# Performance work log

Hardware: AMD Instinct MI355X
Metric: run time of the kernel (lower is better)

The kernel has to match this reference:

```python
import jax, jax.numpy as jnp
import numpy as np

T, H, I, E, K = 4096, 1024, 768, 8, 2

def setup_inputs() -> dict:
    key = jax.random.key(0)
    k1, k2, k3, k4 = jax.random.split(key, 4)
    s_h = 1.0 / np.sqrt(H)
    s_i = 1.0 / np.sqrt(I)
    return {
        "hidden_states": jax.random.normal(k1, (T, H), dtype=jnp.float32),
        "gate_w": jax.random.normal(k2, (E, H), dtype=jnp.float32) * s_h,   # router, fp32
        "w13": jax.random.normal(k3, (E, 2 * I, H), dtype=jnp.float32) * s_h,  # fused gate+up
        "w2": jax.random.normal(k4, (E, H, I), dtype=jnp.float32) * s_i,
        "num_global_tokens": T,
        "max_num_tokens_per_gpu": T,
    }

def reference(hidden_states, gate_w, w13, w2, num_global_tokens, max_num_tokens_per_gpu):
    x = hidden_states  # [T, H]
    orig_dtype = x.dtype
    # router runs in fp32 (router_dtype == 'float32')
    router_logits = jnp.einsum('th,eh->te', x.astype(jnp.float32), gate_w)
    router_logits = router_logits.astype(orig_dtype)
    # FusedMoE top-k: softmax in fp32 over all experts, then top-k; renormalize=False
    probs = jax.nn.softmax(router_logits.astype(jnp.float32), axis=-1)  # [T, E]
    topk_w, topk_ids = jax.lax.top_k(probs, K)  # [T, K]
    # dense combine weights [T, E] (scatter of top-k weights)
    combine = jnp.sum(jax.nn.one_hot(topk_ids, E, dtype=topk_w.dtype) * topk_w[..., None], axis=1)
    combine = combine.astype(orig_dtype)
    # dense per-expert SwiGLU MLP, masked-combined (grouped GEMM reference)
    h = jnp.einsum('th,ejh->tej', x, w13)  # [T, E, 2I]
    g, u = h[..., :I], h[..., I:]
    a = jax.nn.silu(g) * u                 # [T, E, I]
    o = jnp.einsum('tei,ehi->teh', a, w2)  # [T, E, H]
    out = jnp.einsum('teh,te->th', o, combine)  # routed_scaling_factor = 1.0
    return out.reshape(x.shape)
```

## Files before the change

### kernel.cpp

```cpp
#include <hip/hip_runtime.h>
#include <hip/hip_bf16.h>

#define TT 4096
#define HH 1024
#define II 768
#define EE 8
#define TWOI 1536

typedef __attribute__((ext_vector_type(8))) short bf16x8;
typedef __attribute__((ext_vector_type(4))) float f32x4;

__device__ unsigned short g_x_bf[TT * HH];
__device__ unsigned short g_w13_bf[EE * TWOI * HH];
__device__ unsigned short g_w2_bf[EE * HH * II];
__device__ unsigned short g_a[EE * TT * II];
__device__ float g_opart[2 * TT * HH];
__device__ int g_perm_tok[EE * TT];
__device__ float g_perm_w[EE * TT];
__device__ int g_perm_slot[EE * TT];
__device__ int g_cnt[EE];
__device__ int g_e1[TT];
__device__ int g_e2[TT];
__device__ float g_w1f[TT];
__device__ float g_w2f[TT];

__device__ __forceinline__ unsigned short f2bf(float f) {
  union { float f; unsigned u; } v; v.f = f;
  unsigned r = v.u + 0x7fff + ((v.u >> 16) & 1);
  return (unsigned short)(r >> 16);
}

__device__ __forceinline__ void gload16(const void* g, void* l) {
  __builtin_amdgcn_global_load_lds(
      (const __attribute__((address_space(1))) void*)g,
      (__attribute__((address_space(3))) void*)l, 16, 0, 0);
}

__device__ __forceinline__ void cvt_chunks(const float* __restrict__ in,
                                           unsigned short* __restrict__ dst,
                                           int nKB, int chunk) {
  const int lane = threadIdx.x & 63;
  const int r16 = lane & 15, c8 = lane >> 4;
  const int jbg = chunk / nKB, kb = chunk - jbg * nKB;
  const float* src = in + ((size_t)jbg * 16 + r16) * ((size_t)nKB * 32) + kb * 32 + c8 * 8;
  float4 v0 = *(const float4*)(src);
  float4 v1 = *(const float4*)(src + 4);
  ushort4 o0, o1;
  o0.x = f2bf(v0.x); o0.y = f2bf(v0.y); o0.z = f2bf(v0.z); o0.w = f2bf(v0.w);
  o1.x = f2bf(v1.x); o1.y = f2bf(v1.y); o1.z = f2bf(v1.z); o1.w = f2bf(v1.w);
  unsigned short* d = dst + (size_t)chunk * 512 + lane * 8;
  *(ushort4*)(d) = o0;
  *(ushort4*)(d + 4) = o1;
}

__global__ __launch_bounds__(256) void k_prep(const float* __restrict__ x,
                                              const float* __restrict__ gw,
                                              const float* __restrict__ w13) {
  const int b = blockIdx.x;
  const int wv = threadIdx.x >> 6;
  if (b >= 1024) {
    cvt_chunks(w13, g_w13_bf, 32, (b - 1024) * 4 + wv);
    return;
  }
  const int lane = threadIdx.x & 63;
  const int t = b * 4 + wv;

  const float* xr = x + (size_t)t * HH + lane * 16;
  float4 xv0 = *(const float4*)(xr + 0);
  float4 xv1 = *(const float4*)(xr + 4);
  float4 xv2 = *(const float4*)(xr + 8);
  float4 xv3 = *(const float4*)(xr + 12);

  unsigned short* xd = g_x_bf + (size_t)t * HH + lane * 16;
  ushort4 o0, o1, o2, o3;
  o0.x = f2bf(xv0.x); o0.y = f2bf(xv0.y); o0.z = f2bf(xv0.z); o0.w = f2bf(xv0.w);
  o1.x = f2bf(xv1.x); o1.y = f2bf(xv1.y); o1.z = f2bf(xv1.z); o1.w = f2bf(xv1.w);
  o2.x = f2bf(xv2.x); o2.y = f2bf(xv2.y); o2.z = f2bf(xv2.z); o2.w = f2bf(xv2.w);
  o3.x = f2bf(xv3.x); o3.y = f2bf(xv3.y); o3.z = f2bf(xv3.z); o3.w = f2bf(xv3.w);
  *(ushort4*)(xd + 0) = o0;
  *(ushort4*)(xd + 4) = o1;
  *(ushort4*)(xd + 8) = o2;
  *(ushort4*)(xd + 12) = o3;

  float lg[EE];
#pragma unroll
  for (int ei = 0; ei < EE; ++ei) {
    const float* gr = gw + ei * HH + lane * 16;
    float4 g0 = *(const float4*)(gr + 0);
    float4 g1 = *(const float4*)(gr + 4);
    float4 g2 = *(const float4*)(gr + 8);
    float4 g3 = *(const float4*)(gr + 12);
    float a = xv0.x * g0.x + xv0.y * g0.y + xv0.z * g0.z + xv0.w * g0.w
            + xv1.x * g1.x + xv1.y * g1.y + xv1.z * g1.z + xv1.w * g1.w
            + xv2.x * g2.x + xv2.y * g2.y + xv2.z * g2.z + xv2.w * g2.w
            + xv3.x * g3.x + xv3.y * g3.y + xv3.z * g3.z + xv3.w * g3.w;
#pragma unroll
    for (int s = 32; s > 0; s >>= 1) a += __shfl_xor(a, s);
    lg[ei] = a;
  }

  if (lane == 0) {
    float mx = lg[0];
#pragma unroll
    for (int ei = 1; ei < EE; ++ei) mx = fmaxf(mx, lg[ei]);
    float p[EE]; float s = 0.f;
#pragma unroll
    for (int ei = 0; ei < EE; ++ei) { p[ei] = expf(lg[ei] - mx); s += p[ei]; }
    float inv = 1.f / s;
    int e1 = 0; float b1 = lg[0];
#pragma unroll
    for (int ei = 1; ei < EE; ++ei) if (lg[ei] > b1) { b1 = lg[ei]; e1 = ei; }
    int e2 = -1; float b2 = -3.0e38f;
#pragma unroll
    for (int ei = 0; ei < EE; ++ei)
      if (ei != e1 && lg[ei] > b2) { b2 = lg[ei]; e2 = ei; }

    g_e1[t] = e1;
    g_e2[t] = e2;
    g_w1f[t] = p[e1] * inv;
    g_w2f[t] = p[e2] * inv;
  }
}

__global__ __launch_bounds__(256) void k_route2() {
  const int e = blockIdx.x;
  const int tid = threadIdx.x;
  __shared__ int pre[256];

  const int t0 = tid * (TT / 256);
  int c = 0;
#pragma unroll
  for (int j = 0; j < TT / 256; ++j) {
    int t = t0 + j;
    if (g_e1[t] == e) ++c;
    if (g_e2[t] == e) ++c;
  }
  pre[tid] = c;
  __syncthreads();
  for (int off = 1; off < 256; off <<= 1) {
    int v = (tid >= off) ? pre[tid - off] : 0;
    __syncthreads();
    pre[tid] += v;
    __syncthreads();
  }
  int pos = pre[tid] - c;
#pragma unroll
  for (int j = 0; j < TT / 256; ++j) {
    int t = t0 + j;
    if (g_e1[t] == e) {
      g_perm_tok[e * TT + pos] = t;
      g_perm_w[e * TT + pos] = g_w1f[t];
      g_perm_slot[e * TT + pos] = 0;
      ++pos;
    }
    if (g_e2[t] == e) {
      g_perm_tok[e * TT + pos] = t;
      g_perm_w[e * TT + pos] = g_w2f[t];
      g_perm_slot[e * TT + pos] = 1;
      ++pos;
    }
  }
  if (tid == 255) g_cnt[e] = pre[255];
}

__global__ __launch_bounds__(512) void k_gemm1(const float* __restrict__ w2) {
  const int bid = blockIdx.x;
  const int lane = threadIdx.x & 63;
  const int wid = threadIdx.x >> 6;
  if (bid >= 480) {
    int chunk = (bid - 480) * 8 + wid;
    if (chunk < EE * 64 * 24) cvt_chunks(w2, g_w2_bf, 24, chunk);
    return;
  }
  const int e = bid & 7;
  const int k = bid >> 3;
  const int cb = k % 6;
  const int rowbase = (k / 6) * 128;
  const int cnt = g_cnt[e];
  if (rowbase >= cnt) return;
  const int wm = wid >> 1;
  const int wc = wid & 1;

  __shared__ uint4 sA[3][512];
  __shared__ uint4 sBg[3][512];
  __shared__ uint4 sBu[3][512];

  const int r16 = lane & 15;
  const int c8 = lane >> 4;
  const int arow = rowbase + wid * 16 + r16;
  const int tok = (arow < cnt) ? g_perm_tok[e * TT + arow] : 0;
  const unsigned short* aptr = g_x_bf + (size_t)tok * HH + c8 * 8;
  const unsigned short* bgp =
      g_w13_bf + ((size_t)(e * 96 + cb * 8 + wid) * 32) * 512 + lane * 8;
  const unsigned short* bup = bgp + (size_t)48 * 32 * 512;

  const int soff = __builtin_amdgcn_readfirstlane(wid * 1024);

#define STG1(buf, kk) do { \
    gload16(aptr + (kk) * 32, (char*)sA + (buf) * 8192 + soff); \
    gload16(bgp + (size_t)(kk) * 512, (char*)sBg + (buf) * 8192 + soff); \
    gload16(bup + (size_t)(kk) * 512, (char*)sBu + (buf) * 8192 + soff); \
  } while (0)

  f32x4 accg[2][4], accu[2][4];
#pragma unroll
  for (int m = 0; m < 2; ++m)
#pragma unroll
    for (int n = 0; n < 4; ++n) {
      accg[m][n] = (f32x4){0.f, 0.f, 0.f, 0.f};
      accu[m][n] = (f32x4){0.f, 0.f, 0.f, 0.f};
    }

  STG1(0, 0);
  STG1(1, 1);
  for (int ks = 0; ks < 32; ++ks) {
    const int cur = ks % 3;
    if (ks < 30) {
      const int stg = (ks + 2) % 3;
      STG1(stg, ks + 2);
      asm volatile("s_waitcnt vmcnt(6)" ::: "memory");
    } else if (ks == 30) {
      asm volatile("s_waitcnt vmcnt(3)" ::: "memory");
    } else {
      asm volatile("s_waitcnt vmcnt(0)" ::: "memory");
    }
    __builtin_amdgcn_s_barrier();
    __builtin_amdgcn_sched_barrier(0);
    bf16x8 af[2], bgf[4], buf_[4];
#pragma unroll
    for (int m = 0; m < 2; ++m)
      af[m] = *(const bf16x8*)((const char*)sA + cur * 8192 + (wm * 2 + m) * 1024 + lane * 16);
#pragma unroll
    for (int n = 0; n < 4; ++n) {
      int jb = wc * 4 + n;
      bgf[n] = *(const bf16x8*)((const char*)sBg + cur * 8192 + jb * 1024 + lane * 16);
      buf_[n] = *(const bf16x8*)((const char*)sBu + cur * 8192 + jb * 1024 + lane * 16);
    }
#pragma unroll
    for (int m = 0; m < 2; ++m)
#pragma unroll
      for (int n = 0; n < 4; ++n) {
        accg[m][n] = __builtin_amdgcn_mfma_f32_16x16x32_bf16(af[m], bgf[n], accg[m][n], 0, 0, 0);
        accu[m][n] = __builtin_amdgcn_mfma_f32_16x16x32_bf16(af[m], buf_[n], accu[m][n], 0, 0, 0);
      }
    __builtin_amdgcn_sched_barrier(0);
    __builtin_amdgcn_s_barrier();
  }
#undef STG1

  const int rhi = lane >> 4, clo = lane & 15;
  unsigned short* abase = g_a + ((size_t)(e * 256 + (rowbase >> 4)) * 24) * 512;
#pragma unroll
  for (int m = 0; m < 2; ++m) {
#pragma unroll
    for (int jj = 0; jj < 4; ++jj) {
      int rbl = wm * 2 + m;
      int rr = rhi * 4 + jj;
      int row = rowbase + rbl * 16 + rr;
      if (row < cnt) {
#pragma unroll
        for (int n = 0; n < 4; ++n) {
          int kb = cb * 4 + wc * 2 + (n >> 1);
          int sub = (2 * n + (clo >> 3)) & 3;
          float gv = accg[m][n][jj];
          float uv = accu[m][n][jj];
          float av = gv / (1.f + __expf(-gv)) * uv;
          abase[((size_t)rbl * 24 + kb) * 512 + sub * 128 + rr * 8 + (clo & 7)] = f2bf(av);
        }
      }
    }
  }
}

__global__ __launch_bounds__(512) void k_gemm2() {
  const int bid = blockIdx.x;
  const int e = bid & 7;
  const int k = bid >> 3;
  const int cb = k % 8;
  const int rowbase = (k / 8) * 128;
  const int cnt = g_cnt[e];
  if (rowbase >= cnt) return;
  const int tid = threadIdx.x;
  const int lane = tid & 63;
  const int wid = tid >> 6;
  const int wm = wid >> 1;
  const int wc = wid & 1;

  __shared__ uint4 sA[3][512];
  __shared__ uint4 sB[3][512];
  __shared__ int s_tok[128];
  __shared__ float s_w[128];
  __shared__ int s_slot[128];

  if (tid < 128) {
    int row = rowbase + tid;
    bool v = row < cnt;
    s_tok[tid] = v ? g_perm_tok[e * TT + row] : 0;
    s_w[tid] = v ? g_perm_w[e * TT + row] : 0.f;
    s_slot[tid] = v ? g_perm_slot[e * TT + row] : 0;
  }

  const unsigned short* aptr =
      g_a + ((size_t)(e * 256 + (rowbase >> 4) + wid) * 24) * 512 + lane * 8;
  const unsigned short* bp =
      g_w2_bf + ((size_t)(e * 64 + cb * 8 + wid) * 24) * 512 + lane * 8;

  const int soff = __builtin_amdgcn_readfirstlane(wid * 1024);

#define STG2(buf, kk) do { \
    gload16(aptr + (size_t)(kk) * 512, (char*)sA + (buf) * 8192 + soff); \
    gload16(bp + (size_t)(kk) * 512, (char*)sB + (buf) * 8192 + soff); \
  } while (0)

  f32x4 acc[2][4];
#pragma unroll
  for (int m = 0; m < 2; ++m)
#pragma unroll
    for (int n = 0; n < 4; ++n) acc[m][n] = (f32x4){0.f, 0.f, 0.f, 0.f};

  STG2(0, 0);
  STG2(1, 1);
  for (int ks = 0; ks < 24; ++ks) {
    const int cur = ks % 3;
    if (ks < 22) {
      const int stg = (ks + 2) % 3;
      STG2(stg, ks + 2);
      asm volatile("s_waitcnt vmcnt(4)" ::: "memory");
    } else if (ks == 22) {
      asm volatile("s_waitcnt vmcnt(2)" ::: "memory");
    } else {
      asm volatile("s_waitcnt vmcnt(0)" ::: "memory");
    }
    __builtin_amdgcn_s_barrier();
    __builtin_amdgcn_sched_barrier(0);
    bf16x8 af[2], bfr[4];
#pragma unroll
    for (int m = 0; m < 2; ++m)
      af[m] = *(const bf16x8*)((const char*)sA + cur * 8192 + (wm * 2 + m) * 1024 + lane * 16);
#pragma unroll
    for (int n = 0; n < 4; ++n)
      bfr[n] = *(const bf16x8*)((const char*)sB + cur * 8192 + (wc * 4 + n) * 1024 + lane * 16);
#pragma unroll
    for (int m = 0; m < 2; ++m)
#pragma unroll
      for (int n = 0; n < 4; ++n)
        acc[m][n] = __builtin_amdgcn_mfma_f32_16x16x32_bf16(af[m], bfr[n], acc[m][n], 0, 0, 0);
    __builtin_amdgcn_sched_barrier(0);
    __builtin_amdgcn_s_barrier();
  }
#undef STG2

  const int rhi = lane >> 4, clo = lane & 15;
#pragma unroll
  for (int m = 0; m < 2; ++m) {
#pragma unroll
    for (int jj = 0; jj < 4; ++jj) {
      int rloc = wm * 32 + m * 16 + rhi * 4 + jj;
      if (rowbase + rloc < cnt) {
        int tok = s_tok[rloc];
        float w = s_w[rloc];
        float* orow = g_opart + (size_t)s_slot[rloc] * TT * HH + (size_t)tok * HH;
#pragma unroll
        for (int n = 0; n < 4; ++n) {
          int h2 = cb * 128 + wc * 64 + n * 16 + clo;
          orow[h2] = w * acc[m][n][jj];
        }
      }
    }
  }
}

__global__ __launch_bounds__(256) void k_combine(float* __restrict__ out) {
  int idx = (blockIdx.x * 256 + threadIdx.x) * 4;
  float4 p0 = *(const float4*)(g_opart + idx);
  float4 p1 = *(const float4*)(g_opart + TT * HH + idx);
  float4 o;
  o.x = p0.x + p1.x; o.y = p0.y + p1.y; o.z = p0.z + p1.z; o.w = p0.w + p1.w;
  *(float4*)(out + idx) = o;
}

extern "C" void kernel_launch(void* const* d_in, const int* in_sizes, int n_in,
                              void* d_out, int out_size, void* d_ws, size_t ws_size,
                              hipStream_t stream) {
  (void)in_sizes; (void)n_in; (void)d_ws; (void)ws_size; (void)out_size;
  const float* x   = (const float*)d_in[0];
  const float* gw  = (const float*)d_in[1];
  const float* w13 = (const float*)d_in[2];
  const float* w2  = (const float*)d_in[3];
  float* out = (float*)d_out;

  k_prep<<<dim3(7168), dim3(256), 0, stream>>>(x, gw, w13);
  k_route2<<<dim3(EE), dim3(256), 0, stream>>>();
  k_gemm1<<<dim3(480 + 1536), dim3(512), 0, stream>>>(w2);
  k_gemm2<<<dim3(640), dim3(512), 0, stream>>>();
  k_combine<<<dim3(TT * HH / 1024), dim3(256), 0, stream>>>(out);
}
```

Before: 116.0 us.

## Use 4-wave blocks with 64x64 warp tiles and move w2 conversion to prep

```diff
diff --git a/kernel.cpp b/kernel.cpp
--- a/kernel.cpp
+++ b/kernel.cpp
@@ -55,11 +55,13 @@
 
 __global__ __launch_bounds__(256) void k_prep(const float* __restrict__ x,
                                               const float* __restrict__ gw,
-                                              const float* __restrict__ w13) {
+                                              const float* __restrict__ w13,
+                                              const float* __restrict__ w2) {
   const int b = blockIdx.x;
   const int wv = threadIdx.x >> 6;
   if (b >= 1024) {
-    cvt_chunks(w13, g_w13_bf, 32, (b - 1024) * 4 + wv);
+    if (b < 7168) cvt_chunks(w13, g_w13_bf, 32, (b - 1024) * 4 + wv);
+    else          cvt_chunks(w2,  g_w2_bf,  24, (b - 7168) * 4 + wv);
     return;
   }
   const int lane = threadIdx.x & 63;
@@ -163,23 +165,19 @@
   if (tid == 255) g_cnt[e] = pre[255];
 }
 
-__global__ __launch_bounds__(512) void k_gemm1(const float* __restrict__ w2) {
+__global__ __launch_bounds__(256) void k_gemm1() {
   const int bid = blockIdx.x;
-  const int lane = threadIdx.x & 63;
-  const int wid = threadIdx.x >> 6;
-  if (bid >= 480) {
-    int chunk = (bid - 480) * 8 + wid;
-    if (chunk < EE * 64 * 24) cvt_chunks(w2, g_w2_bf, 24, chunk);
-    return;
-  }
   const int e = bid & 7;
   const int k = bid >> 3;
   const int cb = k % 6;
   const int rowbase = (k / 6) * 128;
   const int cnt = g_cnt[e];
   if (rowbase >= cnt) return;
+  const int tid = threadIdx.x;
+  const int lane = tid & 63;
+  const int wid = tid >> 6;
   const int wm = wid >> 1;
-  const int wc = wid & 1;
+  const int wn = wid & 1;
 
   __shared__ uint4 sA[3][512];
   __shared__ uint4 sBg[3][512];
@@ -187,24 +185,34 @@
 
   const int r16 = lane & 15;
   const int c8 = lane >> 4;
-  const int arow = rowbase + wid * 16 + r16;
-  const int tok = (arow < cnt) ? g_perm_tok[e * TT + arow] : 0;
-  const unsigned short* aptr = g_x_bf + (size_t)tok * HH + c8 * 8;
-  const unsigned short* bgp =
+  const int arow0 = rowbase + wid * 16 + r16;
+  const int arow1 = rowbase + (4 + wid) * 16 + r16;
+  const int tok0 = (arow0 < cnt) ? g_perm_tok[e * TT + arow0] : 0;
+  const int tok1 = (arow1 < cnt) ? g_perm_tok[e * TT + arow1] : 0;
+  const unsigned short* aptr0 = g_x_bf + (size_t)tok0 * HH + c8 * 8;
+  const unsigned short* aptr1 = g_x_bf + (size_t)tok1 * HH + c8 * 8;
+  const unsigned short* bgp0 =
       g_w13_bf + ((size_t)(e * 96 + cb * 8 + wid) * 32) * 512 + lane * 8;
-  const unsigned short* bup = bgp + (size_t)48 * 32 * 512;
-
-  const int soff = __builtin_amdgcn_readfirstlane(wid * 1024);
+  const unsigned short* bgp1 =
+      g_w13_bf + ((size_t)(e * 96 + cb * 8 + 4 + wid) * 32) * 512 + lane * 8;
+  const unsigned short* bup0 = bgp0 + (size_t)48 * 32 * 512;
+  const unsigned short* bup1 = bgp1 + (size_t)48 * 32 * 512;
+
+  const int soff0 = __builtin_amdgcn_readfirstlane(wid * 1024);
+  const int soff1 = __builtin_amdgcn_readfirstlane((4 + wid) * 1024);
 
 #define STG1(buf, kk) do { \
-    gload16(aptr + (kk) * 32, (char*)sA + (buf) * 8192 + soff); \
-    gload16(bgp + (size_t)(kk) * 512, (char*)sBg + (buf) * 8192 + soff); \
-    gload16(bup + (size_t)(kk) * 512, (char*)sBu + (buf) * 8192 + soff); \
+    gload16(aptr0 + (kk) * 32, (char*)sA + (buf) * 8192 + soff0); \
+    gload16(aptr1 + (kk) * 32, (char*)sA + (buf) * 8192 + soff1); \
+    gload16(bgp0 + (size_t)(kk) * 512, (char*)sBg + (buf) * 8192 + soff0); \
+    gload16(bgp1 + (size_t)(kk) * 512, (char*)sBg + (buf) * 8192 + soff1); \
+    gload16(bup0 + (size_t)(kk) * 512, (char*)sBu + (buf) * 8192 + soff0); \
+    gload16(bup1 + (size_t)(kk) * 512, (char*)sBu + (buf) * 8192 + soff1); \
   } while (0)
 
-  f32x4 accg[2][4], accu[2][4];
-#pragma unroll
-  for (int m = 0; m < 2; ++m)
+  f32x4 accg[4][4], accu[4][4];
+#pragma unroll
+  for (int m = 0; m < 4; ++m)
 #pragma unroll
     for (int n = 0; n < 4; ++n) {
       accg[m][n] = (f32x4){0.f, 0.f, 0.f, 0.f};
@@ -218,31 +226,33 @@
     if (ks < 30) {
       const int stg = (ks + 2) % 3;
       STG1(stg, ks + 2);
+      asm volatile("s_waitcnt vmcnt(12)" ::: "memory");
+    } else if (ks == 30) {
       asm volatile("s_waitcnt vmcnt(6)" ::: "memory");
-    } else if (ks == 30) {
-      asm volatile("s_waitcnt vmcnt(3)" ::: "memory");
     } else {
       asm volatile("s_waitcnt vmcnt(0)" ::: "memory");
     }
     __builtin_amdgcn_s_barrier();
     __builtin_amdgcn_sched_barrier(0);
-    bf16x8 af[2], bgf[4], buf_[4];
-#pragma unroll
-    for (int m = 0; m < 2; ++m)
-      af[m] = *(const bf16x8*)((const char*)sA + cur * 8192 + (wm * 2 + m) * 1024 + lane * 16);
+    bf16x8 af[4], bgf[4], buf_[4];
+#pragma unroll
+    for (int m = 0; m < 4; ++m)
+      af[m] = *(const bf16x8*)((const char*)sA + cur * 8192 + (wm * 4 + m) * 1024 + lane * 16);
 #pragma unroll
     for (int n = 0; n < 4; ++n) {
-      int jb = wc * 4 + n;
+      int jb = wn * 4 + n;
       bgf[n] = *(const bf16x8*)((const char*)sBg + cur * 8192 + jb * 1024 + lane * 16);
       buf_[n] = *(const bf16x8*)((const char*)sBu + cur * 8192 + jb * 1024 + lane * 16);
     }
-#pragma unroll
-    for (int m = 0; m < 2; ++m)
+    __builtin_amdgcn_s_setprio(1);
+#pragma unroll
+    for (int m = 0; m < 4; ++m)
 #pragma unroll
       for (int n = 0; n < 4; ++n) {
         accg[m][n] = __builtin_amdgcn_mfma_f32_16x16x32_bf16(af[m], bgf[n], accg[m][n], 0, 0, 0);
         accu[m][n] = __builtin_amdgcn_mfma_f32_16x16x32_bf16(af[m], buf_[n], accu[m][n], 0, 0, 0);
       }
+    __builtin_amdgcn_s_setprio(0);
     __builtin_amdgcn_sched_barrier(0);
     __builtin_amdgcn_s_barrier();
   }
@@ -251,16 +261,16 @@
   const int rhi = lane >> 4, clo = lane & 15;
   unsigned short* abase = g_a + ((size_t)(e * 256 + (rowbase >> 4)) * 24) * 512;
 #pragma unroll
-  for (int m = 0; m < 2; ++m) {
+  for (int m = 0; m < 4; ++m) {
 #pragma unroll
     for (int jj = 0; jj < 4; ++jj) {
-      int rbl = wm * 2 + m;
+      int rbl = wm * 4 + m;
       int rr = rhi * 4 + jj;
       int row = rowbase + rbl * 16 + rr;
       if (row < cnt) {
 #pragma unroll
         for (int n = 0; n < 4; ++n) {
-          int kb = cb * 4 + wc * 2 + (n >> 1);
+          int kb = cb * 4 + wn * 2 + (n >> 1);
           int sub = (2 * n + (clo >> 3)) & 3;
           float gv = accg[m][n][jj];
           float uv = accu[m][n][jj];
@@ -272,7 +282,7 @@
   }
 }
 
-__global__ __launch_bounds__(512) void k_gemm2() {
+__global__ __launch_bounds__(256) void k_gemm2() {
   const int bid = blockIdx.x;
   const int e = bid & 7;
   const int k = bid >> 3;
@@ -284,7 +294,7 @@
   const int lane = tid & 63;
   const int wid = tid >> 6;
   const int wm = wid >> 1;
-  const int wc = wid & 1;
+  const int wn = wid & 1;
 
   __shared__ uint4 sA[3][512];
   __shared__ uint4 sB[3][512];
@@ -300,21 +310,28 @@
     s_slot[tid] = v ? g_perm_slot[e * TT + row] : 0;
   }
 
-  const unsigned short* aptr =
+  const unsigned short* aptr0 =
       g_a + ((size_t)(e * 256 + (rowbase >> 4) + wid) * 24) * 512 + lane * 8;
-  const unsigned short* bp =
+  const unsigned short* aptr1 =
+      g_a + ((size_t)(e * 256 + (rowbase >> 4) + 4 + wid) * 24) * 512 + lane * 8;
+  const unsigned short* bp0 =
       g_w2_bf + ((size_t)(e * 64 + cb * 8 + wid) * 24) * 512 + lane * 8;
-
-  const int soff = __builtin_amdgcn_readfirstlane(wid * 1024);
+  const unsigned short* bp1 =
+      g_w2_bf + ((size_t)(e * 64 + cb * 8 + 4 + wid) * 24) * 512 + lane * 8;
+
+  const int soff0 = __builtin_amdgcn_readfirstlane(wid * 1024);
+  const int soff1 = __builtin_amdgcn_readfirstlane((4 + wid) * 1024);
 
 #define STG2(buf, kk) do { \
-    gload16(aptr + (size_t)(kk) * 512, (char*)sA + (buf) * 8192 + soff); \
-    gload16(bp + (size_t)(kk) * 512, (char*)sB + (buf) * 8192 + soff); \
+    gload16(aptr0 + (size_t)(kk) * 512, (char*)sA + (buf) * 8192 + soff0); \
+    gload16(aptr1 + (size_t)(kk) * 512, (char*)sA + (buf) * 8192 + soff1); \
+    gload16(bp0 + (size_t)(kk) * 512, (char*)sB + (buf) * 8192 + soff0); \
+    gload16(bp1 + (size_t)(kk) * 512, (char*)sB + (buf) * 8192 + soff1); \
   } while (0)
 
-  f32x4 acc[2][4];
-#pragma unroll
-  for (int m = 0; m < 2; ++m)
+  f32x4 acc[4][4];
+#pragma unroll
+  for (int m = 0; m < 4; ++m)
 #pragma unroll
     for (int n = 0; n < 4; ++n) acc[m][n] = (f32x4){0.f, 0.f, 0.f, 0.f};
 
@@ -325,26 +342,28 @@
     if (ks < 22) {
       const int stg = (ks + 2) % 3;
       STG2(stg, ks + 2);
+      asm volatile("s_waitcnt vmcnt(8)" ::: "memory");
+    } else if (ks == 22) {
       asm volatile("s_waitcnt vmcnt(4)" ::: "memory");
-    } else if (ks == 22) {
-      asm volatile("s_waitcnt vmcnt(2)" ::: "memory");
     } else {
       asm volatile("s_waitcnt vmcnt(0)" ::: "memory");
     }
     __builtin_amdgcn_s_barrier();
     __builtin_amdgcn_sched_barrier(0);
-    bf16x8 af[2], bfr[4];
-#pragma unroll
-    for (int m = 0; m < 2; ++m)
-      af[m] = *(const bf16x8*)((const char*)sA + cur * 8192 + (wm * 2 + m) * 1024 + lane * 16);
+    bf16x8 af[4], bfr[4];
+#pragma unroll
+    for (int m = 0; m < 4; ++m)
+      af[m] = *(const bf16x8*)((const char*)sA + cur * 8192 + (wm * 4 + m) * 1024 + lane * 16);
 #pragma unroll
     for (int n = 0; n < 4; ++n)
-      bfr[n] = *(const bf16x8*)((const char*)sB + cur * 8192 + (wc * 4 + n) * 1024 + lane * 16);
-#pragma unroll
-    for (int m = 0; m < 2; ++m)
+      bfr[n] = *(const bf16x8*)((const char*)sB + cur * 8192 + (wn * 4 + n) * 1024 + lane * 16);
+    __builtin_amdgcn_s_setprio(1);
+#pragma unroll
+    for (int m = 0; m < 4; ++m)
 #pragma unroll
       for (int n = 0; n < 4; ++n)
         acc[m][n] = __builtin_amdgcn_mfma_f32_16x16x32_bf16(af[m], bfr[n], acc[m][n], 0, 0, 0);
+    __builtin_amdgcn_s_setprio(0);
     __builtin_amdgcn_sched_barrier(0);
     __builtin_amdgcn_s_barrier();
   }
@@ -352,17 +371,17 @@
 
   const int rhi = lane >> 4, clo = lane & 15;
 #pragma unroll
-  for (int m = 0; m < 2; ++m) {
+  for (int m = 0; m < 4; ++m) {
 #pragma unroll
     for (int jj = 0; jj < 4; ++jj) {
-      int rloc = wm * 32 + m * 16 + rhi * 4 + jj;
+      int rloc = wm * 64 + m * 16 + rhi * 4 + jj;
       if (rowbase + rloc < cnt) {
         int tok = s_tok[rloc];
         float w = s_w[rloc];
         float* orow = g_opart + (size_t)s_slot[rloc] * TT * HH + (size_t)tok * HH;
 #pragma unroll
         for (int n = 0; n < 4; ++n) {
-          int h2 = cb * 128 + wc * 64 + n * 16 + clo;
+          int h2 = cb * 128 + wn * 64 + n * 16 + clo;
           orow[h2] = w * acc[m][n][jj];
         }
       }
@@ -389,9 +408,9 @@
   const float* w2  = (const float*)d_in[3];
   float* out = (float*)d_out;
 
-  k_prep<<<dim3(7168), dim3(256), 0, stream>>>(x, gw, w13);
+  k_prep<<<dim3(10240), dim3(256), 0, stream>>>(x, gw, w13, w2);
   k_route2<<<dim3(EE), dim3(256), 0, stream>>>();
-  k_gemm1<<<dim3(480 + 1536), dim3(512), 0, stream>>>(w2);
-  k_gemm2<<<dim3(640), dim3(512), 0, stream>>>();
+  k_gemm1<<<dim3(480), dim3(256), 0, stream>>>();
+  k_gemm2<<<dim3(640), dim3(256), 0, stream>>>();
   k_combine<<<dim3(TT * HH / 1024), dim3(256), 0, stream>>>(out);
 }
```

Result: slower. 150.8 us (+30.0%).

## Move weight bf16 conversions into the routing kernel to overlap with routing

Applied to the files above, without the earlier changes.

```diff
diff --git a/kernel.cpp b/kernel.cpp
--- a/kernel.cpp
+++ b/kernel.cpp
@@ -54,14 +54,9 @@
 }
 
 __global__ __launch_bounds__(256) void k_prep(const float* __restrict__ x,
-                                              const float* __restrict__ gw,
-                                              const float* __restrict__ w13) {
+                                              const float* __restrict__ gw) {
   const int b = blockIdx.x;
   const int wv = threadIdx.x >> 6;
-  if (b >= 1024) {
-    cvt_chunks(w13, g_w13_bf, 32, (b - 1024) * 4 + wv);
-    return;
-  }
   const int lane = threadIdx.x & 63;
   const int t = b * 4 + wv;
 
@@ -122,8 +117,16 @@
   }
 }
 
-__global__ __launch_bounds__(256) void k_route2() {
-  const int e = blockIdx.x;
+__global__ __launch_bounds__(256) void k_mid(const float* __restrict__ w13,
+                                             const float* __restrict__ w2) {
+  const int b = blockIdx.x;
+  const int wv = threadIdx.x >> 6;
+  if (b >= 8) {
+    if (b < 6152) cvt_chunks(w13, g_w13_bf, 32, (b - 8) * 4 + wv);
+    else          cvt_chunks(w2,  g_w2_bf,  24, (b - 6152) * 4 + wv);
+    return;
+  }
+  const int e = b;
   const int tid = threadIdx.x;
   __shared__ int pre[256];
 
@@ -163,21 +166,17 @@
   if (tid == 255) g_cnt[e] = pre[255];
 }
 
-__global__ __launch_bounds__(512) void k_gemm1(const float* __restrict__ w2) {
+__global__ __launch_bounds__(512) void k_gemm1() {
   const int bid = blockIdx.x;
-  const int lane = threadIdx.x & 63;
-  const int wid = threadIdx.x >> 6;
-  if (bid >= 480) {
-    int chunk = (bid - 480) * 8 + wid;
-    if (chunk < EE * 64 * 24) cvt_chunks(w2, g_w2_bf, 24, chunk);
-    return;
-  }
   const int e = bid & 7;
   const int k = bid >> 3;
   const int cb = k % 6;
   const int rowbase = (k / 6) * 128;
   const int cnt = g_cnt[e];
   if (rowbase >= cnt) return;
+  const int tid = threadIdx.x;
+  const int lane = tid & 63;
+  const int wid = tid >> 6;
   const int wm = wid >> 1;
   const int wc = wid & 1;
 
@@ -389,9 +388,9 @@
   const float* w2  = (const float*)d_in[3];
   float* out = (float*)d_out;
 
-  k_prep<<<dim3(7168), dim3(256), 0, stream>>>(x, gw, w13);
-  k_route2<<<dim3(EE), dim3(256), 0, stream>>>();
-  k_gemm1<<<dim3(480 + 1536), dim3(512), 0, stream>>>(w2);
+  k_prep<<<dim3(1024), dim3(256), 0, stream>>>(x, gw);
+  k_mid<<<dim3(9224), dim3(256), 0, stream>>>(w13, w2);
+  k_gemm1<<<dim3(480), dim3(512), 0, stream>>>();
   k_gemm2<<<dim3(640), dim3(512), 0, stream>>>();
   k_combine<<<dim3(TT * HH / 1024), dim3(256), 0, stream>>>(out);
 }
```

Result: no change. 114.5 us (-1.3%).
